# Optimization experiments

Hardware: AMD Instinct MI355X
Metric: run time of the kernel (lower is better)

Reference implementation:

```python
import jax, jax.numpy as jnp
import numpy as np

UNITS = 1024
D_Q = 1024
D_V = 1024


def setup_inputs() -> dict:
    key = jax.random.key(0)
    ks = jax.random.split(key, 8)
    B, S = 32, 2048
    query = jax.random.normal(ks[0], (B, D_Q), dtype=jnp.float32)
    values = jax.random.normal(ks[1], (B, S, D_V), dtype=jnp.float32)
    # Keras Dense params (glorot-ish scale for weights, zero bias init kept random-free)
    W1 = jax.random.normal(ks[2], (D_V, UNITS), dtype=jnp.float32) / np.sqrt(D_V)
    b1 = jnp.zeros((UNITS,), dtype=jnp.float32)
    W2 = jax.random.normal(ks[3], (D_Q, UNITS), dtype=jnp.float32) / np.sqrt(D_Q)
    b2 = jnp.zeros((UNITS,), dtype=jnp.float32)
    V = jax.random.normal(ks[4], (UNITS, 1), dtype=jnp.float32) / np.sqrt(UNITS)
    bV = jnp.zeros((1,), dtype=jnp.float32)
    return {"query": query, "values": values, "W1": W1, "b1": b1,
            "W2": W2, "b2": b2, "V": V, "bV": bV}


def reference(query, values, W1, b1, W2, b2, V, bV):
    # query: [B, d_q], values: [B, S, d_v]
    proj_v = jnp.einsum('bsd,du->bsu', values, W1) + b1        # [B, S, U]
    proj_q = (query @ W2 + b2)[:, None, :]                      # [B, 1, U]
    score = jnp.tanh(proj_v + proj_q) @ V + bV                  # [B, S, 1]
    attention_weights = jax.nn.softmax(score, axis=1)           # [B, S, 1]
    context_vector = jnp.sum(attention_weights * values, axis=1)  # [B, d_v]
    return (context_vector, attention_weights)
```

## Files before the change

kernel.cpp:

```cpp
#include <hip/hip_runtime.h>
#include <math.h>

#define B_  32
#define S_  2048
#define DV  1024
#define U_  1024

typedef __attribute__((ext_vector_type(8))) short bf16x8;
typedef __attribute__((ext_vector_type(4))) float f32x4;

__device__ inline unsigned short f2bf(float f) {
    unsigned int x = __float_as_uint(f);
    return (unsigned short)((x + 0x7fffu + ((x >> 16) & 1u)) >> 16);
}

__device__ inline float tanh_fast(float x) {
    float ax = fabsf(x);
    float e  = __expf(ax + ax);
    float t  = 1.0f - __fdividef(2.0f, e + 1.0f);
    return copysignf(t, x);
}

__device__ __forceinline__ void gload16(const void* g, void* l) {
    __builtin_amdgcn_global_load_lds(
        (const __attribute__((address_space(1))) void*)g,
        (__attribute__((address_space(3))) void*)l,
        16, 0, 0);
}

__global__ void init_kernel(const float* __restrict__ b1, const float* __restrict__ b2,
                            float* __restrict__ t, float* __restrict__ ctx,
                            float* __restrict__ scores) {
    int i = blockIdx.x * 256 + threadIdx.x;
    scores[i] = 0.f;
    if (i < B_ * U_) {
        int u = i & (U_ - 1);
        t[i]   = b1[u] + b2[u];
        ctx[i] = 0.f;
    }
}

__global__ void projq_kernel(const float* __restrict__ q, const float* __restrict__ W2,
                             float* __restrict__ t) {
    int b  = blockIdx.x;
    int ks = blockIdx.y;
    int tid = threadIdx.x;
    __shared__ float qs[256];
    qs[tid] = q[b * DV + ks * 256 + tid];
    __syncthreads();
    float a0 = 0.f, a1 = 0.f, a2 = 0.f, a3 = 0.f;
    const float* w = W2 + (size_t)(ks * 256) * U_;
    for (int d = 0; d < 256; ++d) {
        float qd = qs[d];
        const float* wr = w + (size_t)d * U_ + tid;
        a0 += qd * wr[0];
        a1 += qd * wr[256];
        a2 += qd * wr[512];
        a3 += qd * wr[768];
    }
    atomicAdd(&t[b * U_ + tid      ], a0);
    atomicAdd(&t[b * U_ + tid + 256], a1);
    atomicAdd(&t[b * U_ + tid + 512], a2);
    atomicAdd(&t[b * U_ + tid + 768], a3);
}

__global__ void cvt_values(const float* __restrict__ v, unsigned short* __restrict__ o) {
    size_t i = ((size_t)blockIdx.x * 256 + threadIdx.x) * 8;
    float4 f0 = *(const float4*)(v + i);
    float4 f1 = *(const float4*)(v + i + 4);
    union { unsigned short s[8]; uint4 u; } p;
    p.s[0] = f2bf(f0.x); p.s[1] = f2bf(f0.y); p.s[2] = f2bf(f0.z); p.s[3] = f2bf(f0.w);
    p.s[4] = f2bf(f1.x); p.s[5] = f2bf(f1.y); p.s[6] = f2bf(f1.z); p.s[7] = f2bf(f1.w);
    *(uint4*)(o + i) = p.u;
}

__global__ void prep_w1t(const float* __restrict__ W1, unsigned short* __restrict__ W1T) {
    __shared__ float tile[64][65];
    int k0 = blockIdx.x * 64, u0 = blockIdx.y * 64;
    int t = threadIdx.x;
    int lr = t >> 4, lc = (t & 15) * 4;
#pragma unroll
    for (int i = 0; i < 4; ++i) {
        float4 f = *(const float4*)&W1[(size_t)(k0 + lr + i * 16) * U_ + u0 + lc];
        tile[lr + i * 16][lc + 0] = f.x; tile[lr + i * 16][lc + 1] = f.y;
        tile[lr + i * 16][lc + 2] = f.z; tile[lr + i * 16][lc + 3] = f.w;
    }
    __syncthreads();
    int ur = t >> 2, kq = (t & 3) * 16;
    union { unsigned short s[8]; uint4 u; } p0, p1;
#pragma unroll
    for (int e = 0; e < 8; ++e) p0.s[e] = f2bf(tile[kq + e][ur]);
#pragma unroll
    for (int e = 0; e < 8; ++e) p1.s[e] = f2bf(tile[kq + 8 + e][ur]);
    unsigned short* dst = W1T + (size_t)(u0 + ur) * 1024 + k0 + kq;
    *(uint4*)dst       = p0.u;
    *(uint4*)(dst + 8) = p1.u;
}

__launch_bounds__(256, 2)
__global__ void scores_mfma2(const unsigned short* __restrict__ Abf,
                             const unsigned short* __restrict__ W1T,
                             const float* __restrict__ tvec,
                             const float* __restrict__ V,
                             float* __restrict__ scores) {
    __shared__ unsigned short sA[2 * 128 * 64];
    __shared__ unsigned short sB[2 * 64 * 64];

    const int tid  = threadIdx.x;
    const int lane = tid & 63;
    const int wave = tid >> 6;
    const int wm   = wave & 1;
    const int wn   = wave >> 1;
    const int l15  = lane & 15;
    const int lq   = lane >> 4;

    const int id    = blockIdx.x;
    const int utile = (id >> 3) & 7;
    const int stile = (id & 7) | ((id >> 6) << 3);
    const size_t row0 = (size_t)stile * 256;
    const int b       = (int)(row0 >> 11);
    const int s_local = (int)(row0 & 2047);
    const int u0      = utile * 128;

    const unsigned short* aS[4];
    const unsigned short* bS[2];
    char* aD[4];
    char* bD[2];
#pragma unroll
    for (int j = 0; j < 4; ++j) {
        int L = j * 4096 + tid * 16;
        int line = L >> 7, p = (L >> 4) & 7;
        int c = p ^ (line & 7);
        int row = line * 2 + (c >> 2);
        int kq = c & 3;
        aS[j] = Abf + (row0 + row) * 1024 + kq * 8;
        aD[j] = (char*)sA + j * 4096 + wave * 1024;
    }
#pragma unroll
    for (int j = 0; j < 2; ++j) {
        int L = j * 4096 + tid * 16;
        int line = L >> 7, p = (L >> 4) & 7;
        int c = p ^ (line & 7);
        int row = line * 2 + (c >> 2);
        int kq = c & 3;
        bS[j] = W1T + (size_t)(u0 + row) * 1024 + kq * 8;
        bD[j] = (char*)sB + j * 4096 + wave * 1024;
    }

    const int prd = ((l15 & 1) * 4 + lq) ^ ((l15 >> 1) & 7);
    const unsigned short* paBase = sA + (wm * 64 + (l15 >> 1)) * 64 + prd * 8;
    const unsigned short* pbBase = sB + (wn * 32 + (l15 >> 1)) * 64 + prd * 8;

    f32x4 acc[8][4];
#pragma unroll
    for (int m = 0; m < 8; ++m)
#pragma unroll
        for (int n = 0; n < 4; ++n) acc[m][n] = (f32x4)0.f;

#pragma unroll
    for (int j = 0; j < 4; ++j) gload16(aS[j], aD[j]);
#pragma unroll
    for (int j = 0; j < 2; ++j) gload16(bS[j], bD[j]);
#pragma unroll
    for (int j = 0; j < 4; ++j) aS[j] += 32;
#pragma unroll
    for (int j = 0; j < 2; ++j) bS[j] += 32;
    __syncthreads();

    for (int kt = 0; kt < 32; ++kt) {
        const int cur = kt & 1;
        if (kt < 31) {
            const int nb = cur ^ 1;
#pragma unroll
            for (int j = 0; j < 4; ++j) gload16(aS[j], aD[j] + nb * 16384);
#pragma unroll
            for (int j = 0; j < 2; ++j) gload16(bS[j], bD[j] + nb * 8192);
#pragma unroll
            for (int j = 0; j < 4; ++j) aS[j] += 32;
#pragma unroll
            for (int j = 0; j < 2; ++j) bS[j] += 32;
        }
        const unsigned short* pa = paBase + cur * 8192;
        const unsigned short* pb = pbBase + cur * 4096;
        bf16x8 af[8], bfr[4];
#pragma unroll
        for (int m = 0; m < 8; ++m) af[m] = *(const bf16x8*)(pa + m * 512);
#pragma unroll
        for (int n = 0; n < 4; ++n) bfr[n] = *(const bf16x8*)(pb + n * 512);
        __builtin_amdgcn_s_setprio(1);
#pragma unroll
        for (int n = 0; n < 4; ++n)
#pragma unroll
            for (int m = 0; m < 8; ++m)
                acc[m][n] = __builtin_amdgcn_mfma_f32_16x16x32_bf16(af[m], bfr[n], acc[m][n], 0, 0, 0);
        __builtin_amdgcn_s_setprio(0);
        __syncthreads();
    }

    float* fscore = (float*)sA;
    fscore[tid] = 0.f;
    __syncthreads();
    float tu[4], vu[4];
#pragma unroll
    for (int n = 0; n < 4; ++n) {
        int u = u0 + wn * 64 + n * 16 + l15;
        tu[n] = tvec[b * U_ + u];
        vu[n] = V[u];
    }
#pragma unroll
    for (int m = 0; m < 8; ++m) {
#pragma unroll
        for (int r = 0; r < 4; ++r) {
            float p = 0.f;
#pragma unroll
            for (int n = 0; n < 4; ++n) p += tanh_fast(acc[m][n][r] + tu[n]) * vu[n];
            p += __shfl_xor(p, 1);
            p += __shfl_xor(p, 2);
            p += __shfl_xor(p, 4);
            p += __shfl_xor(p, 8);
            if (l15 == 0) atomicAdd(&fscore[wm * 128 + m * 16 + lq * 4 + r], p);
        }
    }
    __syncthreads();
    atomicAdd(&scores[(size_t)b * S_ + s_local + tid], fscore[tid]);
}

template<bool ABF16>
__launch_bounds__(256, 2)
__global__ void scores_mfma(const void* __restrict__ aPtr,
                            const unsigned short* __restrict__ W1T,
                            const float* __restrict__ t,
                            const float* __restrict__ V,
                            float* __restrict__ scores) {
    __shared__ unsigned short sA[128 * 40];
    __shared__ unsigned short sB[256 * 40];
    __shared__ float fscore[128];

    const int tid  = threadIdx.x;
    const int lane = tid & 63;
    const int wave = tid >> 6;
    const int wm = wave & 1, wn = wave >> 1;
    const int l15 = lane & 15, lq = lane >> 4;

    const int id    = blockIdx.x;
    const int utile = (id >> 3) & 3;
    const int stile = (id & 7) | ((id >> 5) << 3);
    const size_t row0 = (size_t)stile * 128;
    const int b       = (int)(row0 >> 11);
    const int s_local = (int)(row0 & 2047);
    const int u0      = utile * 256;

    if (tid < 128) fscore[tid] = 0.f;

    const int ar = tid >> 1, ak = (tid & 1) << 4;
    const int br = tid >> 1, bk = (tid & 1) << 4;

    const float* Af = (const float*)aPtr + (row0 + ar) * 1024 + ak;
    const unsigned short* Ab = (const unsigned short*)aPtr + (row0 + ar) * 1024 + ak;
    const unsigned short* Bp0 = W1T + (size_t)(u0 + br) * 1024 + bk;
    const unsigned short* Bp1 = Bp0 + 128 * 1024;

    f32x4 acc[4][8];
#pragma unroll
    for (int i = 0; i < 4; ++i)
#pragma unroll
        for (int j = 0; j < 8; ++j) acc[i][j] = (f32x4)0.f;

    uint4 sa0, sa1, sb0, sb1, sb2, sb3;
    float4 fa0, fa1, fa2, fa3;

    if (ABF16) {
        sa0 = *(const uint4*)(Ab);
        sa1 = *(const uint4*)(Ab + 8);
    } else {
        fa0 = *(const float4*)(Af);
        fa1 = *(const float4*)(Af + 4);
        fa2 = *(const float4*)(Af + 8);
        fa3 = *(const float4*)(Af + 12);
    }
    sb0 = *(const uint4*)(Bp0);
    sb1 = *(const uint4*)(Bp0 + 8);
    sb2 = *(const uint4*)(Bp1);
    sb3 = *(const uint4*)(Bp1 + 8);

    for (int k0 = 0; k0 < 1024; k0 += 32) {
        __syncthreads();
        if (ABF16) {
            *(uint4*)&sA[ar * 40 + ak]     = sa0;
            *(uint4*)&sA[ar * 40 + ak + 8] = sa1;
        } else {
            union { unsigned short s[8]; uint4 u; } p0, p1;
            p0.s[0] = f2bf(fa0.x); p0.s[1] = f2bf(fa0.y); p0.s[2] = f2bf(fa0.z); p0.s[3] = f2bf(fa0.w);
            p0.s[4] = f2bf(fa1.x); p0.s[5] = f2bf(fa1.y); p0.s[6] = f2bf(fa1.z); p0.s[7] = f2bf(fa1.w);
            p1.s[0] = f2bf(fa2.x); p1.s[1] = f2bf(fa2.y); p1.s[2] = f2bf(fa2.z); p1.s[3] = f2bf(fa2.w);
            p1.s[4] = f2bf(fa3.x); p1.s[5] = f2bf(fa3.y); p1.s[6] = f2bf(fa3.z); p1.s[7] = f2bf(fa3.w);
            *(uint4*)&sA[ar * 40 + ak]     = p0.u;
            *(uint4*)&sA[ar * 40 + ak + 8] = p1.u;
        }
        *(uint4*)&sB[br * 40 + bk]           = sb0;
        *(uint4*)&sB[br * 40 + bk + 8]       = sb1;
        *(uint4*)&sB[(br + 128) * 40 + bk]     = sb2;
        *(uint4*)&sB[(br + 128) * 40 + bk + 8] = sb3;

        if (k0 + 32 < 1024) {
            int nk = k0 + 32;
            if (ABF16) {
                sa0 = *(const uint4*)(Ab + nk);
                sa1 = *(const uint4*)(Ab + nk + 8);
            } else {
                fa0 = *(const float4*)(Af + nk);
                fa1 = *(const float4*)(Af + nk + 4);
                fa2 = *(const float4*)(Af + nk + 8);
                fa3 = *(const float4*)(Af + nk + 12);
            }
            sb0 = *(const uint4*)(Bp0 + nk);
            sb1 = *(const uint4*)(Bp0 + nk + 8);
            sb2 = *(const uint4*)(Bp1 + nk);
            sb3 = *(const uint4*)(Bp1 + nk + 8);
        }
        __syncthreads();

        bf16x8 af[4];
#pragma unroll
        for (int i = 0; i < 4; ++i)
            af[i] = *(const bf16x8*)&sA[(64 * wm + 16 * i + l15) * 40 + lq * 8];
#pragma unroll
        for (int j = 0; j < 8; ++j) {
            bf16x8 bfj = *(const bf16x8*)&sB[(128 * wn + 16 * j + l15) * 40 + lq * 8];
#pragma unroll
            for (int i = 0; i < 4; ++i)
                acc[i][j] = __builtin_amdgcn_mfma_f32_16x16x32_bf16(af[i], bfj, acc[i][j], 0, 0, 0);
        }
    }

    float tu[8], vu[8];
#pragma unroll
    for (int j = 0; j < 8; ++j) {
        int u = u0 + 128 * wn + 16 * j + l15;
        tu[j] = t[b * U_ + u];
        vu[j] = V[u];
    }
#pragma unroll
    for (int i = 0; i < 4; ++i) {
#pragma unroll
        for (int r = 0; r < 4; ++r) {
            float p = 0.f;
#pragma unroll
            for (int j = 0; j < 8; ++j) p += tanh_fast(acc[i][j][r] + tu[j]) * vu[j];
            p += __shfl_xor(p, 1);
            p += __shfl_xor(p, 2);
            p += __shfl_xor(p, 4);
            p += __shfl_xor(p, 8);
            if (l15 == 0) atomicAdd(&fscore[64 * wm + 16 * i + lq * 4 + r], p);
        }
    }
    __syncthreads();
    if (tid < 128) atomicAdd(&scores[(size_t)b * S_ + s_local + tid], fscore[tid]);
}

__launch_bounds__(256, 2)
__global__ void scores_vec(const float* __restrict__ values, const float* __restrict__ W1,
                           const float* __restrict__ t, const float* __restrict__ V,
                           float* __restrict__ scores) {
    __shared__ float vA[16][132];
    __shared__ float vB[16][68];
    __shared__ float fscore[128];
    const int b   = blockIdx.y;
    const int s0  = blockIdx.x * 128;
    const int tid = threadIdx.x;
    const int tx  = tid & 15, ty = tid >> 4;
    if (tid < 128) fscore[tid] = 0.f;
    const float* vbase = values + ((size_t)b * S_ + s0) * (size_t)DV;
    const int lm = tid >> 2, lkq = (tid & 3) * 4;
    const int lbk = tid >> 4, lbj = (tid & 15) * 4;
    for (int nt = 0; nt < U_ / 64; ++nt) {
        const int u0 = nt * 64;
        float acc[8][4];
#pragma unroll
        for (int i = 0; i < 8; ++i)
#pragma unroll
            for (int j = 0; j < 4; ++j) acc[i][j] = 0.f;
        for (int k0 = 0; k0 < DV; k0 += 16) {
            __syncthreads();
            const float4 v0 = *(const float4*)(vbase + (size_t)lm * DV + k0 + lkq);
            const float4 v1 = *(const float4*)(vbase + (size_t)(lm + 64) * DV + k0 + lkq);
            vA[lkq + 0][lm] = v0.x; vA[lkq + 1][lm] = v0.y;
            vA[lkq + 2][lm] = v0.z; vA[lkq + 3][lm] = v0.w;
            vA[lkq + 0][lm + 64] = v1.x; vA[lkq + 1][lm + 64] = v1.y;
            vA[lkq + 2][lm + 64] = v1.z; vA[lkq + 3][lm + 64] = v1.w;
            *(float4*)&vB[lbk][lbj] = *(const float4*)(W1 + (size_t)(k0 + lbk) * U_ + u0 + lbj);
            __syncthreads();
#pragma unroll
            for (int k = 0; k < 16; ++k) {
                float4 va0 = *(const float4*)&vA[k][ty * 8];
                float4 va1 = *(const float4*)&vA[k][ty * 8 + 4];
                float4 vb  = *(const float4*)&vB[k][tx * 4];
                float a_[8] = {va0.x, va0.y, va0.z, va0.w, va1.x, va1.y, va1.z, va1.w};
                float b_[4] = {vb.x, vb.y, vb.z, vb.w};
#pragma unroll
                for (int i = 0; i < 8; ++i)
#pragma unroll
                    for (int j = 0; j < 4; ++j) acc[i][j] += a_[i] * b_[j];
            }
        }
        float tq[4], vv[4];
#pragma unroll
        for (int j = 0; j < 4; ++j) {
            int u = u0 + tx * 4 + j;
            tq[j] = t[b * U_ + u];
            vv[j] = V[u];
        }
#pragma unroll
        for (int i = 0; i < 8; ++i) {
            float p = 0.f;
#pragma unroll
            for (int j = 0; j < 4; ++j) p += tanhf(acc[i][j] + tq[j]) * vv[j];
            p += __shfl_down(p, 8, 16);
            p += __shfl_down(p, 4, 16);
            p += __shfl_down(p, 2, 16);
            p += __shfl_down(p, 1, 16);
            if (tx == 0) fscore[ty * 8 + i] += p;
        }
    }
    __syncthreads();
    if (tid < 128) scores[(size_t)b * S_ + s0 + tid] = fscore[tid];
}

__global__ void softmax_kernel(const float* __restrict__ scores, float* __restrict__ wout) {
    int b = blockIdx.x;
    int tid = threadIdx.x;
    __shared__ float red[256];
    float v[8];
    float m = -1e30f;
#pragma unroll
    for (int i = 0; i < 8; ++i) {
        v[i] = scores[(size_t)b * S_ + tid + i * 256];
        m = fmaxf(m, v[i]);
    }
    red[tid] = m; __syncthreads();
    for (int off = 128; off > 0; off >>= 1) {
        if (tid < off) red[tid] = fmaxf(red[tid], red[tid + off]);
        __syncthreads();
    }
    m = red[0];
    __syncthreads();
    float s = 0.f;
#pragma unroll
    for (int i = 0; i < 8; ++i) { v[i] = __expf(v[i] - m); s += v[i]; }
    red[tid] = s; __syncthreads();
    for (int off = 128; off > 0; off >>= 1) {
        if (tid < off) red[tid] += red[tid + off];
        __syncthreads();
    }
    float inv = 1.f / red[0];
#pragma unroll
    for (int i = 0; i < 8; ++i) wout[(size_t)b * S_ + tid + i * 256] = v[i] * inv;
}

__global__ void context_kernel(const float* __restrict__ values, const float* __restrict__ w,
                               float* __restrict__ ctx) {
    int b  = blockIdx.x;
    int dc = blockIdx.y;
    int sc = blockIdx.z;
    int tid = threadIdx.x;
    int d = dc * 256 + tid;
    __shared__ float ws_[256];
    ws_[tid] = w[(size_t)b * S_ + sc * 256 + tid];
    __syncthreads();
    float acc = 0.f;
    const float* vp = values + ((size_t)b * S_ + sc * 256) * (size_t)DV + d;
#pragma unroll 4
    for (int s = 0; s < 256; ++s) acc += ws_[s] * vp[(size_t)s * DV];
    atomicAdd(&ctx[b * DV + d], acc);
}

extern "C" void kernel_launch(void* const* d_in, const int* in_sizes, int n_in,
                              void* d_out, int out_size, void* d_ws, size_t ws_size,
                              hipStream_t stream) {
    const float* query  = (const float*)d_in[0];
    const float* values = (const float*)d_in[1];
    const float* W1     = (const float*)d_in[2];
    const float* b1     = (const float*)d_in[3];
    const float* W2     = (const float*)d_in[4];
    const float* b2     = (const float*)d_in[5];
    const float* V      = (const float*)d_in[6];

    float* out  = (float*)d_out;
    float* ctx  = out;
    float* wout = out + B_ * DV;

    char* ws = (char*)d_ws;
    const size_t W1T_BYTES = (size_t)U_ * DV * 2;
    const size_t T_BYTES   = (size_t)B_ * U_ * 4;
    const size_t SC_BYTES  = (size_t)B_ * S_ * 4;
    const size_t ABF_BYTES = (size_t)B_ * S_ * DV * 2;

    if (ws_size >= W1T_BYTES + T_BYTES + SC_BYTES + ABF_BYTES) {
        unsigned short* W1T = (unsigned short*)ws;
        float* t      = (float*)(ws + W1T_BYTES);
        float* scores = t + B_ * U_;
        unsigned short* Abf = (unsigned short*)(scores + B_ * S_);

        init_kernel   <<<dim3(256),      256, 0, stream>>>(b1, b2, t, ctx, scores);
        projq_kernel  <<<dim3(32, 4),    256, 0, stream>>>(query, W2, t);
        cvt_values    <<<dim3(32768),    256, 0, stream>>>(values, Abf);
        prep_w1t      <<<dim3(16, 16),   256, 0, stream>>>(W1, W1T);
        scores_mfma2  <<<dim3(2048),     256, 0, stream>>>(Abf, W1T, t, V, scores);
        softmax_kernel<<<dim3(32),       256, 0, stream>>>(scores, wout);
        context_kernel<<<dim3(32, 4, 8), 256, 0, stream>>>(values, wout, ctx);
    } else if (ws_size >= W1T_BYTES + T_BYTES + SC_BYTES) {
        unsigned short* W1T = (unsigned short*)ws;
        float* t      = (float*)(ws + W1T_BYTES);
        float* scores = t + B_ * U_;

        init_kernel   <<<dim3(256),      256, 0, stream>>>(b1, b2, t, ctx, scores);
        projq_kernel  <<<dim3(32, 4),    256, 0, stream>>>(query, W2, t);
        prep_w1t      <<<dim3(16, 16),   256, 0, stream>>>(W1, W1T);
        scores_mfma<false><<<dim3(2048), 256, 0, stream>>>(values, W1T, t, V, scores);
        softmax_kernel<<<dim3(32),       256, 0, stream>>>(scores, wout);
        context_kernel<<<dim3(32, 4, 8), 256, 0, stream>>>(values, wout, ctx);
    } else {
        float* t      = (float*)ws;
        float* scores = t + B_ * U_;

        init_kernel   <<<dim3(256),      256, 0, stream>>>(b1, b2, t, ctx, scores);
        projq_kernel  <<<dim3(32, 4),    256, 0, stream>>>(query, W2, t);
        scores_vec    <<<dim3(16, 32),   256, 0, stream>>>(values, W1, t, V, scores);
        softmax_kernel<<<dim3(32),       256, 0, stream>>>(scores, wout);
        context_kernel<<<dim3(32, 4, 8), 256, 0, stream>>>(values, wout, ctx);
    }
}
```

Before: 644.9 us.

## Triple-buffer MFMA scores GEMM loads and split projq over more blocks

The scores GEMM moves from a double-buffered to a triple-buffered LDS pipeline, with two tiles prefetched ahead. It uses explicit vmcnt waits and raw s_barrier instead of __syncthreads, so the global-to-LDS loads have more time to land before they are consumed. LDS use per block grows to 72 KB, which may limit occupancy at two blocks per CU. Separately, projq_kernel splits its reduction dimension into 16 chunks of 64 instead of 4 chunks of 256, giving more parallelism at the cost of more atomics.

```diff
diff --git a/kernel.cpp b/kernel.cpp
--- a/kernel.cpp
+++ b/kernel.cpp
@@ -45,12 +45,12 @@
     int b  = blockIdx.x;
     int ks = blockIdx.y;
     int tid = threadIdx.x;
-    __shared__ float qs[256];
-    qs[tid] = q[b * DV + ks * 256 + tid];
+    __shared__ float qs[64];
+    if (tid < 64) qs[tid] = q[b * DV + ks * 64 + tid];
     __syncthreads();
     float a0 = 0.f, a1 = 0.f, a2 = 0.f, a3 = 0.f;
-    const float* w = W2 + (size_t)(ks * 256) * U_;
-    for (int d = 0; d < 256; ++d) {
+    const float* w = W2 + (size_t)(ks * 64) * U_;
+    for (int d = 0; d < 64; ++d) {
         float qd = qs[d];
         const float* wr = w + (size_t)d * U_ + tid;
         a0 += qd * wr[0];
@@ -98,13 +98,13 @@
 }
 
 __launch_bounds__(256, 2)
-__global__ void scores_mfma2(const unsigned short* __restrict__ Abf,
+__global__ void scores_mfma3(const unsigned short* __restrict__ Abf,
                              const unsigned short* __restrict__ W1T,
                              const float* __restrict__ tvec,
                              const float* __restrict__ V,
                              float* __restrict__ scores) {
-    __shared__ unsigned short sA[2 * 128 * 64];
-    __shared__ unsigned short sB[2 * 64 * 64];
+    __shared__ unsigned short sA[3 * 8192];
+    __shared__ unsigned short sB[3 * 4096];
 
     const int tid  = threadIdx.x;
     const int lane = tid & 63;
@@ -165,23 +165,35 @@
     for (int j = 0; j < 4; ++j) aS[j] += 32;
 #pragma unroll
     for (int j = 0; j < 2; ++j) bS[j] += 32;
-    __syncthreads();
+#pragma unroll
+    for (int j = 0; j < 4; ++j) gload16(aS[j], aD[j] + 16384);
+#pragma unroll
+    for (int j = 0; j < 2; ++j) gload16(bS[j], bD[j] + 8192);
+#pragma unroll
+    for (int j = 0; j < 4; ++j) aS[j] += 32;
+#pragma unroll
+    for (int j = 0; j < 2; ++j) bS[j] += 32;
+    __builtin_amdgcn_sched_barrier(0);
+    asm volatile("s_waitcnt vmcnt(6)" ::: "memory");
+    __builtin_amdgcn_s_barrier();
+    __builtin_amdgcn_sched_barrier(0);
+
+    int cb = 0;
+    int sb = 2;
 
     for (int kt = 0; kt < 32; ++kt) {
-        const int cur = kt & 1;
-        if (kt < 31) {
-            const int nb = cur ^ 1;
-#pragma unroll
-            for (int j = 0; j < 4; ++j) gload16(aS[j], aD[j] + nb * 16384);
-#pragma unroll
-            for (int j = 0; j < 2; ++j) gload16(bS[j], bD[j] + nb * 8192);
+        if (kt < 30) {
+#pragma unroll
+            for (int j = 0; j < 4; ++j) gload16(aS[j], aD[j] + sb * 16384);
+#pragma unroll
+            for (int j = 0; j < 2; ++j) gload16(bS[j], bD[j] + sb * 8192);
 #pragma unroll
             for (int j = 0; j < 4; ++j) aS[j] += 32;
 #pragma unroll
             for (int j = 0; j < 2; ++j) bS[j] += 32;
         }
-        const unsigned short* pa = paBase + cur * 8192;
-        const unsigned short* pb = pbBase + cur * 4096;
+        const unsigned short* pa = paBase + cb * 8192;
+        const unsigned short* pb = pbBase + cb * 4096;
         bf16x8 af[8], bfr[4];
 #pragma unroll
         for (int m = 0; m < 8; ++m) af[m] = *(const bf16x8*)(pa + m * 512);
@@ -194,7 +206,18 @@
             for (int m = 0; m < 8; ++m)
                 acc[m][n] = __builtin_amdgcn_mfma_f32_16x16x32_bf16(af[m], bfr[n], acc[m][n], 0, 0, 0);
         __builtin_amdgcn_s_setprio(0);
-        __syncthreads();
+
+        __builtin_amdgcn_sched_barrier(0);
+        if (kt < 30) {
+            asm volatile("s_waitcnt vmcnt(6)" ::: "memory");
+        } else if (kt == 30) {
+            asm volatile("s_waitcnt vmcnt(0)" ::: "memory");
+        }
+        __builtin_amdgcn_s_barrier();
+        __builtin_amdgcn_sched_barrier(0);
+
+        cb = (cb == 2) ? 0 : cb + 1;
+        sb = (sb == 2) ? 0 : sb + 1;
     }
 
     float* fscore = (float*)sA;
@@ -502,10 +525,10 @@
         unsigned short* Abf = (unsigned short*)(scores + B_ * S_);
 
         init_kernel   <<<dim3(256),      256, 0, stream>>>(b1, b2, t, ctx, scores);
-        projq_kernel  <<<dim3(32, 4),    256, 0, stream>>>(query, W2, t);
+        projq_kernel  <<<dim3(32, 16),   256, 0, stream>>>(query, W2, t);
         cvt_values    <<<dim3(32768),    256, 0, stream>>>(values, Abf);
         prep_w1t      <<<dim3(16, 16),   256, 0, stream>>>(W1, W1T);
-        scores_mfma2  <<<dim3(2048),     256, 0, stream>>>(Abf, W1T, t, V, scores);
+        scores_mfma3  <<<dim3(2048),     256, 0, stream>>>(Abf, W1T, t, V, scores);
         softmax_kernel<<<dim3(32),       256, 0, stream>>>(scores, wout);
         context_kernel<<<dim3(32, 4, 8), 256, 0, stream>>>(values, wout, ctx);
     } else if (ws_size >= W1T_BYTES + T_BYTES + SC_BYTES) {
@@ -514,7 +537,7 @@
         float* scores = t + B_ * U_;
 
         init_kernel   <<<dim3(256),      256, 0, stream>>>(b1, b2, t, ctx, scores);
-        projq_kernel  <<<dim3(32, 4),    256, 0, stream>>>(query, W2, t);
+        projq_kernel  <<<dim3(32, 16),   256, 0, stream>>>(query, W2, t);
         prep_w1t      <<<dim3(16, 16),   256, 0, stream>>>(W1, W1T);
         scores_mfma<false><<<dim3(2048), 256, 0, stream>>>(values, W1T, t, V, scores);
         softmax_kernel<<<dim3(32),       256, 0, stream>>>(scores, wout);
@@ -524,7 +547,7 @@
         float* scores = t + B_ * U_;
 
         init_kernel   <<<dim3(256),      256, 0, stream>>>(b1, b2, t, ctx, scores);
-        projq_kernel  <<<dim3(32, 4),    256, 0, stream>>>(query, W2, t);
+        projq_kernel  <<<dim3(32, 16),   256, 0, stream>>>(query, W2, t);
         scores_vec    <<<dim3(16, 32),   256, 0, stream>>>(values, W1, t, V, scores);
         softmax_kernel<<<dim3(32),       256, 0, stream>>>(scores, wout);
         context_kernel<<<dim3(32, 4, 8), 256, 0, stream>>>(values, wout, ctx);
```

Result: no change. 634.7 us (-1.6%).
